# Performance work log

Hardware: AMD Instinct MI355X
Metric: run time of the kernel (lower is better)

## Reference

```python
import jax, jax.numpy as jnp
import numpy as np
from jax import lax

B, N, D = 2, 2048, 1024
H = 16
DH = D // H
EXP = 4
INNER = EXP * D
KS = 3
POWER = 2
LN_EPS = 1e-5


def _layer_norm(x, g, b):
    mu = jnp.mean(x, axis=-1, keepdims=True)
    var = jnp.mean(jnp.square(x - mu), axis=-1, keepdims=True)
    return (x - mu) * lax.rsqrt(var + LN_EPS) * g + b


def setup_inputs() -> dict:
    key = jax.random.key(0)
    ks = jax.random.split(key, 12)
    s = 1.0 / np.sqrt(D)
    si = 1.0 / np.sqrt(INNER)
    return {
        "Q_in": jax.random.normal(ks[0], (B, N, D), jnp.float32),
        "X": jax.random.normal(ks[1], (B, N, D), jnp.float32),
        "Wq": jax.random.normal(ks[2], (D, D), jnp.float32) * s,
        "Wk": jax.random.normal(ks[3], (D, D), jnp.float32) * s,
        "Wv": jax.random.normal(ks[4], (D, D), jnp.float32) * s,
        "Wo": jax.random.normal(ks[5], (D, D), jnp.float32) * s,
        "Wup": jax.random.normal(ks[6], (D, 2 * INNER), jnp.float32) * s,
        "conv_w": jax.random.normal(ks[7], (INNER, 1, KS), jnp.float32) * 0.5,
        "Wdown": jax.random.normal(ks[8], (INNER, D), jnp.float32) * si,
        "g1": jnp.ones((D,), jnp.float32),
        "b1": jnp.zeros((D,), jnp.float32),
        "g2": jnp.ones((D,), jnp.float32),
        "b2": jnp.zeros((D,), jnp.float32),
        "dt": jnp.float32(0.1),
    }


def reference(Q_in, X, Wq, Wk, Wv, Wo, Wup, conv_w, Wdown, g1, b1, g2, b2, dt):
    Bn, Nn, d = Q_in.shape
    # --- attention path: kernelized quadratic attention (relu^power) ---
    Hc = _layer_norm(Q_in, g1, b1) + X                     # [B,N,d]
    def heads(x):
        return x.reshape(Bn, Nn, H, DH).transpose(0, 2, 1, 3)  # [B,H,N,dh]
    Qp = heads(Hc @ Wq)
    Kp = heads(Hc @ Wk)
    Vp = heads(Hc @ Wv)
    PhiQ = jax.nn.elu(Qp) + 1.0
    PhiK = jax.nn.elu(Kp) + 1.0
    W = jnp.einsum("bhnd,bhmd->bhnm", PhiQ, PhiK)          # [B,H,N,N]
    W = jnp.maximum(W, 0.0) ** POWER
    Attr = jnp.einsum("bhnm,bhmd->bhnd", W, Vp)
    Norm = jnp.sum(W, axis=-1, keepdims=True) + 1.0
    m = Attr / Norm - Vp                                   # [B,H,N,dh]
    m_concat = m.transpose(0, 2, 1, 3).reshape(Bn, Nn, d)
    dt_safe = jax.nn.softplus(dt)
    Q_interact = Q_in + dt_safe * (m_concat @ Wo)
    # --- gated depthwise-conv FFN (ConvSwiGLU) ---
    Qn2 = _layer_norm(Q_interact, g2, b2)
    GU = Qn2 @ Wup                                         # [B,N,2*INNER]
    G, U = GU[..., :INNER], GU[..., INNER:]
    Hf = jax.nn.silu(G) * U                                # [B,N,INNER]
    Hf_t = Hf.transpose(0, 2, 1)                           # [B,INNER,N]
    pad = (KS - 1) // 2
    Hc_t = lax.conv_general_dilated(
        Hf_t, conv_w, window_strides=(1,), padding=[(pad, pad)],
        dimension_numbers=("NCH", "OIH", "NCH"), feature_group_count=INNER)
    H_out = Hc_t.transpose(0, 2, 1) @ Wdown
    return Q_interact + H_out
```

## Files before the change

### kernel.cpp

```cpp
#include <hip/hip_runtime.h>

typedef unsigned short u16;
typedef __attribute__((ext_vector_type(8))) __bf16 bf16x8;
typedef __attribute__((ext_vector_type(4))) float f32x4;
typedef __attribute__((ext_vector_type(8))) unsigned short us8v;

__device__ __forceinline__ u16 f2bf(float x){
  union { float f; unsigned u; } v; v.f = x;
  unsigned r = v.u + 0x7fffu + ((v.u >> 16) & 1u);
  return (u16)(r >> 16);
}
__device__ __forceinline__ float bf2f(u16 h){
  union { unsigned u; float f; } v; v.u = ((unsigned)h) << 16;
  return v.f;
}
__device__ __forceinline__ void gld16(const void* g, void* l){
  __builtin_amdgcn_global_load_lds((const __attribute__((address_space(1))) unsigned int*)g,
                                   (__attribute__((address_space(3))) unsigned int*)l, 16, 0, 0);
}

__global__ __launch_bounds__(256) void tr_all(
    const float* __restrict__ Wq, const float* __restrict__ Wk,
    const float* __restrict__ Wv, const float* __restrict__ Wo,
    const float* __restrict__ Wup, const float* __restrict__ Wdown,
    u16* __restrict__ WqkvT, u16* __restrict__ WoT,
    u16* __restrict__ WupT, u16* __restrict__ WdT,
    const float* __restrict__ Qin, const float* __restrict__ X,
    const float* __restrict__ g1, const float* __restrict__ b1,
    u16* __restrict__ HcB)
{
  __shared__ float t[32][33];
  int tx = threadIdx.x, ty = threadIdx.y;
  int id = blockIdx.x;
  if (id >= 16384){
    int row = id - 16384, tid = ty*32 + tx;
    const float4 x = ((const float4*)(Qin + (size_t)row*1024))[tid];
    float s = x.x + x.y + x.z + x.w;
    float sq = x.x*x.x + x.y*x.y + x.z*x.z + x.w*x.w;
    #pragma unroll
    for (int o=32;o>0;o>>=1){ s += __shfl_xor(s, o); sq += __shfl_xor(sq, o); }
    __shared__ float ss[4], ssq[4];
    int wid = tid>>6;
    if ((tid&63)==0){ ss[wid]=s; ssq[wid]=sq; }
    __syncthreads();
    s = ss[0]+ss[1]+ss[2]+ss[3]; sq = ssq[0]+ssq[1]+ssq[2]+ssq[3];
    float mu = s*(1.0f/1024.0f);
    float var = sq*(1.0f/1024.0f) - mu*mu;
    float rstd = rsqrtf(var + 1e-5f);
    float4 xx = ((const float4*)(X + (size_t)row*1024))[tid];
    float4 gv = ((const float4*)g1)[tid];
    float4 bv = ((const float4*)b1)[tid];
    ushort4 o;
    o.x = f2bf((x.x-mu)*rstd*gv.x + bv.x + xx.x);
    o.y = f2bf((x.y-mu)*rstd*gv.y + bv.y + xx.y);
    o.z = f2bf((x.z-mu)*rstd*gv.z + bv.z + xx.z);
    o.w = f2bf((x.w-mu)*rstd*gv.w + bv.w + xx.w);
    ((ushort4*)(HcB + (size_t)row*1024))[tid] = o;
    return;
  }
  if (id < 4096){
    int w = id >> 10, b = id & 1023;
    int c0 = (b & 31)*32, r0 = (b >> 5)*32;
    const float* S = (w==0)?Wq:(w==1)?Wk:(w==2)?Wv:Wo;
    u16* D = (w==3)? WoT : (WqkvT + (size_t)w*1024*1024);
    #pragma unroll
    for (int j=0;j<32;j+=8) t[ty+j][tx] = S[(size_t)(r0+ty+j)*1024 + (c0+tx)];
    __syncthreads();
    #pragma unroll
    for (int j=0;j<32;j+=8) D[(size_t)(c0+ty+j)*1024 + (r0+tx)] = f2bf(t[tx][ty+j]);
  } else if (id < 12288){
    int b = id - 4096;
    int c0 = (b & 255)*32, r0 = (b >> 8)*32;
    #pragma unroll
    for (int j=0;j<32;j+=8) t[ty+j][tx] = Wup[(size_t)(r0+ty+j)*8192 + (c0+tx)];
    __syncthreads();
    #pragma unroll
    for (int j=0;j<32;j+=8){
      int c = c0 + ty + j;
      int rdst = (c < 4096) ? ((c>>4)*32 + (c&15)) : (((c-4096)>>4)*32 + 16 + (c&15));
      WupT[(size_t)rdst*1024 + (r0+tx)] = f2bf(t[tx][ty+j]);
    }
  } else {
    int b = id - 12288;
    int c0 = (b & 31)*32, r0 = (b >> 5)*32;
    #pragma unroll
    for (int j=0;j<32;j+=8) t[ty+j][tx] = Wdown[(size_t)(r0+ty+j)*1024 + (c0+tx)];
    __syncthreads();
    #pragma unroll
    for (int j=0;j<32;j+=8) WdT[(size_t)(c0+ty+j)*4096 + (r0+tx)] = f2bf(t[tx][ty+j]);
  }
}

__global__ __launch_bounds__(256) void ln2_kernel(const u16* __restrict__ P,
    const float* __restrict__ Qin, const float* __restrict__ dtp,
    const float* __restrict__ g, const float* __restrict__ b,
    float* __restrict__ Qint, u16* __restrict__ Qn2){
  int row = blockIdx.x, tid = threadIdx.x;
  float sp = log1pf(__expf(dtp[0]));
  size_t off = (size_t)row*1024;
  ushort4 p0 = ((const ushort4*)(P + off))[tid];
  ushort4 p1 = ((const ushort4*)(P + 4194304 + off))[tid];
  float4 q  = ((const float4*)(Qin + off))[tid];
  float4 x;
  x.x = q.x + sp*(bf2f(p0.x)+bf2f(p1.x)); x.y = q.y + sp*(bf2f(p0.y)+bf2f(p1.y));
  x.z = q.z + sp*(bf2f(p0.z)+bf2f(p1.z)); x.w = q.w + sp*(bf2f(p0.w)+bf2f(p1.w));
  ((float4*)(Qint + off))[tid] = x;
  float s = x.x + x.y + x.z + x.w;
  float sq = x.x*x.x + x.y*x.y + x.z*x.z + x.w*x.w;
  #pragma unroll
  for (int o=32;o>0;o>>=1){ s += __shfl_xor(s, o); sq += __shfl_xor(sq, o); }
  __shared__ float ss[4], ssq[4];
  int wid = tid>>6;
  if ((tid&63)==0){ ss[wid]=s; ssq[wid]=sq; }
  __syncthreads();
  s = ss[0]+ss[1]+ss[2]+ss[3]; sq = ssq[0]+ssq[1]+ssq[2]+ssq[3];
  float mu = s*(1.0f/1024.0f);
  float var = sq*(1.0f/1024.0f) - mu*mu;
  float rstd = rsqrtf(var + 1e-5f);
  float4 gv = ((const float4*)g)[tid];
  float4 bv = ((const float4*)b)[tid];
  ushort4 o;
  o.x = f2bf((x.x-mu)*rstd*gv.x + bv.x);
  o.y = f2bf((x.y-mu)*rstd*gv.y + bv.y);
  o.z = f2bf((x.z-mu)*rstd*gv.z + bv.z);
  o.w = f2bf((x.w-mu)*rstd*gv.w + bv.w);
  ((ushort4*)(Qn2 + off))[tid] = o;
}

__global__ __launch_bounds__(256, 3) void gemm_qkv(
    const u16* __restrict__ A, const u16* __restrict__ Bt, void* __restrict__ Op)
{
  __shared__ u16 As[128*64];
  __shared__ u16 Bs[128*64];
  const int tid = threadIdx.x, wid = tid>>6, lane = tid&63;
  const int g = lane>>4, l = lane&15, l7 = l&7;
  const int row0 = blockIdx.x*128, col0 = blockIdx.y*128;
  const int wr = (wid&1)*64, wc = (wid>>1)*64;
  f32x4 acc[4][4] = {};
  for (int k0 = 0; k0 < 1024; k0 += 64){
    __syncthreads();
    #pragma unroll
    for (int i=0;i<4;i++){
      int ch0 = i*256 + wid*64;
      int ch = ch0 + lane;
      int r = ch >> 3, c = ch & 7;
      int cs = c ^ (r & 7);
      gld16(A  + (size_t)(row0+r)*1024 + k0 + cs*8, (char*)As + ch0*16);
      gld16(Bt + (size_t)(col0+r)*1024 + k0 + cs*8, (char*)Bs + ch0*16);
    }
    __syncthreads();
    #pragma unroll
    for (int kk=0; kk<2; kk++){
      bf16x8 a[4], b[4];
      #pragma unroll
      for (int i=0;i<4;i++) a[i] = *(const bf16x8*)(As + (wr + i*16 + l)*64 + (((kk*4+g)^l7)*8));
      #pragma unroll
      for (int j=0;j<4;j++) b[j] = *(const bf16x8*)(Bs + (wc + j*16 + l)*64 + (((kk*4+g)^l7)*8));
      #pragma unroll
      for (int i=0;i<4;i++)
        #pragma unroll
        for (int j=0;j<4;j++)
          acc[i][j] = __builtin_amdgcn_mfma_f32_16x16x32_bf16(a[i], b[j], acc[i][j], 0, 0, 0);
    }
  }
  u16* P = (u16*)Op;
  #pragma unroll
  for (int i=0;i<4;i++)
   #pragma unroll
   for (int j=0;j<4;j++){
     int col = col0 + wc + j*16 + l;
     int qk = col >> 10, c = col & 1023;
     int h = c >> 6, d = c & 63;
     int rowb = row0 + wr + i*16 + g*4;
     int bb = rowb >> 11, n = rowb & 2047;
     if (qk == 2){
       ushort4 vs;
       vs.x = f2bf(acc[i][j][0]); vs.y = f2bf(acc[i][j][1]);
       vs.z = f2bf(acc[i][j][2]); vs.w = f2bf(acc[i][j][3]);
       *(ushort4*)(P + (size_t)8388608 + (((size_t)(bb*16 + h))*64 + d)*2048 + n) = vs;
     } else {
       #pragma unroll
       for (int r=0;r<4;r++){
         float v = acc[i][j][r];
         float phi = v > 0.f ? v + 1.f : __expf(v);
         P[(size_t)qk*4194304 + (((size_t)(bb*16 + h))*2048 + (n+r))*64 + d] = f2bf(phi);
       }
     }
   }
}

__global__ __launch_bounds__(256, 2) void gemm_wide_up(
    const u16* __restrict__ A, const u16* __restrict__ Bt, u16* __restrict__ Op)
{
  __shared__ u16 As[256*64];
  __shared__ u16 Bs[128*64];
  const int tid = threadIdx.x, wid = tid>>6, lane = tid&63;
  const int g = lane>>4, l = lane&15, l7 = l&7;
  const int bid = blockIdx.x;
  const int bx = bid & 15;
  const int by = (bid>>7)*8 + ((bid>>4) & 7);
  const int row0 = bx*256, col0 = by*128;
  const int wr = (wid&1)*128, wc = (wid>>1)*64;
  f32x4 acc[8][4] = {};
  for (int k0 = 0; k0 < 1024; k0 += 64){
    __syncthreads();
    #pragma unroll
    for (int i=0;i<8;i++){
      int ch0 = i*256 + wid*64;
      int ch = ch0 + lane;
      int r = ch >> 3, c = ch & 7;
      int cs = c ^ (r & 7);
      gld16(A + (size_t)(row0+r)*1024 + k0 + cs*8, (char*)As + ch0*16);
    }
    #pragma unroll
    for (int i=0;i<4;i++){
      int ch0 = i*256 + wid*64;
      int ch = ch0 + lane;
      int r = ch >> 3, c = ch & 7;
      int cs = c ^ (r & 7);
      gld16(Bt + (size_t)(col0+r)*1024 + k0 + cs*8, (char*)Bs + ch0*16);
    }
    __syncthreads();
    #pragma unroll
    for (int kk=0; kk<2; kk++){
      bf16x8 a[8], b[4];
      #pragma unroll
      for (int i=0;i<8;i++) a[i] = *(const bf16x8*)(As + (wr + i*16 + l)*64 + (((kk*4+g)^l7)*8));
      #pragma unroll
      for (int j=0;j<4;j++) b[j] = *(const bf16x8*)(Bs + (wc + j*16 + l)*64 + (((kk*4+g)^l7)*8));
      #pragma unroll
      for (int i=0;i<8;i++)
        #pragma unroll
        for (int j=0;j<4;j++)
          acc[i][j] = __builtin_amdgcn_mfma_f32_16x16x32_bf16(a[i], b[j], acc[i][j], 0, 0, 0);
    }
  }
  #pragma unroll
  for (int i=0;i<8;i++)
   #pragma unroll
   for (int jj=0;jj<4;jj+=2)
    #pragma unroll
    for (int r=0;r<4;r++){
      int row = row0 + wr + i*16 + g*4 + r;
      int pair = (col0 + wc + jj*16) >> 5;
      float G = acc[i][jj][r], U = acc[i][jj+1][r];
      float hf = G/(1.f+__expf(-G))*U;
      Op[(size_t)row*4096 + pair*16 + l] = f2bf(hf);
    }
}

__global__ __launch_bounds__(256, 3) void gemm_part(
    const u16* __restrict__ A, const u16* __restrict__ Bt,
    int Nc, int K, int Ks, u16* __restrict__ Op)
{
  __shared__ u16 As[128*64];
  __shared__ u16 Bs[128*64];
  const int tid = threadIdx.x, wid = tid>>6, lane = tid&63;
  const int g = lane>>4, l = lane&15, l7 = l&7;
  const int row0 = blockIdx.x*128, col0 = blockIdx.y*128;
  const int kbase = blockIdx.z*Ks;
  const int wr = (wid&1)*64, wc = (wid>>1)*64;
  f32x4 acc[4][4] = {};
  for (int k0 = kbase; k0 < kbase + Ks; k0 += 64){
    __syncthreads();
    #pragma unroll
    for (int i=0;i<4;i++){
      int ch0 = i*256 + wid*64;
      int ch = ch0 + lane;
      int r = ch >> 3, c = ch & 7;
      int cs = c ^ (r & 7);
      gld16(A  + (size_t)(row0+r)*K + k0 + cs*8, (char*)As + ch0*16);
      gld16(Bt + (size_t)(col0+r)*K + k0 + cs*8, (char*)Bs + ch0*16);
    }
    __syncthreads();
    #pragma unroll
    for (int kk=0; kk<2; kk++){
      bf16x8 a[4], b[4];
      #pragma unroll
      for (int i=0;i<4;i++) a[i] = *(const bf16x8*)(As + (wr + i*16 + l)*64 + (((kk*4+g)^l7)*8));
      #pragma unroll
      for (int j=0;j<4;j++) b[j] = *(const bf16x8*)(Bs + (wc + j*16 + l)*64 + (((kk*4+g)^l7)*8));
      #pragma unroll
      for (int i=0;i<4;i++)
        #pragma unroll
        for (int j=0;j<4;j++)
          acc[i][j] = __builtin_amdgcn_mfma_f32_16x16x32_bf16(a[i], b[j], acc[i][j], 0, 0, 0);
    }
  }
  u16* P = Op + (size_t)blockIdx.z*4194304;
  #pragma unroll
  for (int i=0;i<4;i++)
   #pragma unroll
   for (int j=0;j<4;j++)
    #pragma unroll
    for (int r=0;r<4;r++){
      int row = row0 + wr + i*16 + g*4 + r;
      int col = col0 + wc + j*16 + l;
      P[(size_t)row*Nc + col] = f2bf(acc[i][j][r]);
    }
}

__global__ __launch_bounds__(256) void reduce_out(const float* __restrict__ Qint,
    const u16* __restrict__ P, float* __restrict__ out){
  size_t i = (size_t)blockIdx.x*256 + threadIdx.x;
  float4 a  = ((const float4*)Qint)[i];
  ushort4 p0 = ((const ushort4*)P)[i];
  ushort4 p1 = ((const ushort4*)(P + 4194304))[i];
  float4 o;
  o.x = a.x + bf2f(p0.x) + bf2f(p1.x); o.y = a.y + bf2f(p0.y) + bf2f(p1.y);
  o.z = a.z + bf2f(p0.z) + bf2f(p1.z); o.w = a.w + bf2f(p0.w) + bf2f(p1.w);
  ((float4*)out)[i] = o;
}

__global__ __launch_bounds__(256, 2) void attn_kernel(
    const u16* __restrict__ PhiQ, const u16* __restrict__ PhiK,
    const u16* __restrict__ Vt, u16* __restrict__ Mb)
{
  __shared__ u16 sK[2][128][32];
  __shared__ u16 sV[4][64][32];
  __shared__ u16 sW[128*128];
  const int tid = threadIdx.x, wid = tid>>6, lane = tid&63;
  const int g = lane>>4, l = lane&15;
  const int l3 = l & 3;
  const int q0 = blockIdx.x*128, bh = blockIdx.y;
  const u16* Q  = PhiQ + (size_t)bh*2048*64;
  const u16* Kb = PhiK + (size_t)bh*2048*64;
  const u16* V  = Vt   + (size_t)bh*64*2048;
  bf16x8 bq[8][2];
  #pragma unroll
  for (int ct=0;ct<8;ct++)
    #pragma unroll
    for (int ks=0;ks<2;ks++)
      bq[ct][ks] = *(const bf16x8*)(Q + (size_t)(q0 + ct*16 + l)*64 + ks*32 + g*8);
  f32x4 accO[2][4] = {};
  float rsum[8] = {0.f,0.f,0.f,0.f,0.f,0.f,0.f,0.f};
  for (int m0 = 0; m0 < 2048; m0 += 128){
    __syncthreads();
    #pragma unroll
    for (int ks=0; ks<2; ks++)
      #pragma unroll
      for (int i=0;i<2;i++){
        int ch0 = i*256 + wid*64;
        int ch = ch0 + lane;
        int r = ch >> 2, q = ch & 3;
        int qs = q ^ (r & 3);
        gld16(Kb + (size_t)(m0+r)*64 + ks*32 + qs*8, (char*)&sK[ks][0][0] + ch0*16);
      }
    #pragma unroll
    for (int c=0; c<4; c++){
      int ch0 = wid*64;
      int ch = ch0 + lane;
      int d = ch >> 2, q = ch & 3;
      int qs = q ^ (d & 3);
      gld16(V + (size_t)d*2048 + m0 + c*32 + qs*8, (char*)&sV[c][0][0] + ch0*16);
    }
    __syncthreads();
    f32x4 st[2][8] = {};
    bf16x8 ak[2][2];
    #pragma unroll
    for (int rt=0;rt<2;rt++)
      #pragma unroll
      for (int ks=0;ks<2;ks++)
        ak[rt][ks] = *(const bf16x8*)&sK[ks][wid*32 + rt*16 + l][(g^l3)*8];
    #pragma unroll
    for (int ct=0;ct<8;ct++){
      #pragma unroll
      for (int ks=0;ks<2;ks++){
        st[0][ct] = __builtin_amdgcn_mfma_f32_16x16x32_bf16(ak[0][ks], bq[ct][ks], st[0][ct], 0,0,0);
        st[1][ct] = __builtin_amdgcn_mfma_f32_16x16x32_bf16(ak[1][ks], bq[ct][ks], st[1][ct], 0,0,0);
      }
    }
    #pragma unroll
    for (int ct=0;ct<8;ct++){
      float part = 0.f;
      #pragma unroll
      for (int rt=0;rt<2;rt++){
        float s0 = fmaxf(st[rt][ct][0], 0.f), s1 = fmaxf(st[rt][ct][1], 0.f);
        float s2 = fmaxf(st[rt][ct][2], 0.f), s3 = fmaxf(st[rt][ct][3], 0.f);
        float w0 = s0*s0, w1 = s1*s1, w2 = s2*s2, w3 = s3*s3;
        part += w0 + w1 + w2 + w3;
        int n = ct*16 + l;
        int mblk = wid*4 + rt*2 + (g>>1);
        ushort4 w4;
        w4.x = f2bf(w0); w4.y = f2bf(w1); w4.z = f2bf(w2); w4.w = f2bf(w3);
        *(ushort4*)(sW + n*128 + ((mblk ^ l)*8) + (g&1)*4) = w4;
      }
      rsum[ct] += part;
    }
    __syncthreads();
    #pragma unroll
    for (int ks=0;ks<4;ks++){
      int n0 = wid*32 + l, n1 = wid*32 + 16 + l;
      bf16x8 aw0 = *(const bf16x8*)(sW + n0*128 + (((ks*4+g) ^ (n0&15))*8));
      bf16x8 aw1 = *(const bf16x8*)(sW + n1*128 + (((ks*4+g) ^ (n1&15))*8));
      #pragma unroll
      for (int ct=0;ct<4;ct++){
        bf16x8 bv = *(const bf16x8*)&sV[ks][ct*16 + l][(g^l3)*8];
        accO[0][ct] = __builtin_amdgcn_mfma_f32_16x16x32_bf16(aw0, bv, accO[0][ct], 0,0,0);
        accO[1][ct] = __builtin_amdgcn_mfma_f32_16x16x32_bf16(aw1, bv, accO[1][ct], 0,0,0);
      }
    }
  }
  __syncthreads();
  float* sRS = (float*)sW;
  float* sNorm = ((float*)sW) + 512;
  #pragma unroll
  for (int ct=0;ct<8;ct++){
    float v = rsum[ct];
    v += __shfl_xor(v, 16);
    v += __shfl_xor(v, 32);
    rsum[ct] = v;
  }
  if (g == 0){
    #pragma unroll
    for (int ct=0;ct<8;ct++) sRS[wid*128 + ct*16 + l] = rsum[ct];
  }
  __syncthreads();
  if (tid < 128) sNorm[tid] = sRS[tid] + sRS[128+tid] + sRS[256+tid] + sRS[384+tid] + 1.0f;
  __syncthreads();
  const int bb = bh >> 4, h = bh & 15;
  #pragma unroll
  for (int rt=0;rt<2;rt++)
   #pragma unroll
   for (int ct=0;ct<4;ct++)
    #pragma unroll
    for (int r=0;r<4;r++){
      int n = wid*32 + rt*16 + g*4 + r;
      int d = ct*16 + l;
      float norm = sNorm[n];
      float vv = bf2f(V[(size_t)d*2048 + q0 + n]);
      float mv = accO[rt][ct][r]/norm - vv;
      Mb[((size_t)(bb*2048) + q0 + n)*1024 + h*64 + d] = f2bf(mv);
    }
}

__global__ __launch_bounds__(256) void conv_kernel(const u16* __restrict__ Hf, const float* __restrict__ w,
                                                   u16* __restrict__ Cv){
  int row = blockIdx.y;
  int n = row & 2047;
  int c0 = (blockIdx.x*256 + threadIdx.x)*8;
  us8v h0 = {0,0,0,0,0,0,0,0}, h2 = {0,0,0,0,0,0,0,0};
  us8v h1 = *(const us8v*)(Hf + (size_t)row*4096 + c0);
  if (n > 0)    h0 = *(const us8v*)(Hf + (size_t)(row-1)*4096 + c0);
  if (n < 2047) h2 = *(const us8v*)(Hf + (size_t)(row+1)*4096 + c0);
  us8v o;
  #pragma unroll
  for (int e=0;e<8;e++){
    int c = c0 + e;
    float acc = bf2f(h0[e])*w[c*3+0] + bf2f(h1[e])*w[c*3+1] + bf2f(h2[e])*w[c*3+2];
    o[e] = f2bf(acc);
  }
  *(us8v*)(Cv + (size_t)row*4096 + c0) = o;
}

extern "C" void kernel_launch(void* const* d_in, const int* in_sizes, int n_in,
                              void* d_out, int out_size, void* d_ws, size_t ws_size,
                              hipStream_t stream)
{
  const float* Q_in  = (const float*)d_in[0];
  const float* X     = (const float*)d_in[1];
  const float* Wq    = (const float*)d_in[2];
  const float* Wk    = (const float*)d_in[3];
  const float* Wv    = (const float*)d_in[4];
  const float* Wo    = (const float*)d_in[5];
  const float* Wup   = (const float*)d_in[6];
  const float* convw = (const float*)d_in[7];
  const float* Wdown = (const float*)d_in[8];
  const float* g1    = (const float*)d_in[9];
  const float* b1    = (const float*)d_in[10];
  const float* g2    = (const float*)d_in[11];
  const float* b2    = (const float*)d_in[12];
  const float* dt    = (const float*)d_in[13];
  float* out = (float*)d_out;

  char* ws = (char*)d_ws;
  const size_t MB = (size_t)1 << 20;
  u16* HcB   = (u16*)(ws + 0*MB);
  u16* WqkvT = (u16*)(ws + 8*MB);
  u16* WoT   = (u16*)(ws + 14*MB);
  u16* PhiQ  = (u16*)(ws + 16*MB);
  u16* Vt    = (u16*)(ws + 32*MB);
  u16* Mb    = (u16*)(ws + 40*MB);
  u16* Po    = (u16*)(ws + 48*MB);
  u16* WupT  = (u16*)(ws + 80*MB);
  u16* WdT   = (u16*)(ws + 96*MB);
  float* Qint = (float*)(ws + 104*MB);
  u16* Qn2   = (u16*)(ws + 120*MB);
  u16* Hf    = (u16*)(ws + 0*MB);
  u16* Cv    = (u16*)(ws + 40*MB);
  u16* Pd    = (u16*)(ws + 0*MB);
  u16* PhiK  = PhiQ + 4194304;

  tr_all<<<20480, dim3(32, 8), 0, stream>>>(Wq, Wk, Wv, Wo, Wup, Wdown,
                                            WqkvT, WoT, WupT, WdT,
                                            Q_in, X, g1, b1, HcB);

  gemm_qkv<<<dim3(32, 24), 256, 0, stream>>>(HcB, WqkvT, PhiQ);

  attn_kernel<<<dim3(16, 32), 256, 0, stream>>>(PhiQ, PhiK, Vt, Mb);

  gemm_part<<<dim3(32, 8, 2), 256, 0, stream>>>(Mb, WoT, 1024, 1024, 512, Po);

  ln2_kernel<<<4096, 256, 0, stream>>>(Po, Q_in, dt, g2, b2, Qint, Qn2);

  gemm_wide_up<<<1024, 256, 0, stream>>>(Qn2, WupT, Hf);

  conv_kernel<<<dim3(2, 4096), 256, 0, stream>>>(Hf, convw, Cv);

  gemm_part<<<dim3(32, 8, 2), 256, 0, stream>>>(Cv, WdT, 1024, 4096, 2048, Pd);
  reduce_out<<<4096, 256, 0, stream>>>(Qint, Pd, out);
}
```

Baseline: 407.9 us.

## Double-buffer the up-projection GEMM with a 256x256 tile and 512 threads

Reworks the gate/up GEMM to use 512-thread blocks computing 256x256 output tiles. The A and B tiles are double-buffered in LDS, with staggered global-to-LDS prefetches and explicit vmcnt waits, so loads overlap MFMA work instead of sitting between two barriers. It also remaps block ids across XCDs and raises wave priority around the MFMA section. The change targets memory latency and barrier stalls, at the cost of 128KB of LDS per block, which limits occupancy to one block per CU.

```diff
diff --git a/kernel.cpp b/kernel.cpp
--- a/kernel.cpp
+++ b/kernel.cpp
@@ -189,52 +189,78 @@
    }
 }
 
-__global__ __launch_bounds__(256, 2) void gemm_wide_up(
+__global__ __launch_bounds__(512, 2) void gemm_wide_up(
     const u16* __restrict__ A, const u16* __restrict__ Bt, u16* __restrict__ Op)
 {
-  __shared__ u16 As[256*64];
-  __shared__ u16 Bs[128*64];
+  __shared__ __attribute__((aligned(16))) u16 As[2][256*64];
+  __shared__ __attribute__((aligned(16))) u16 Bs[2][256*64];
   const int tid = threadIdx.x, wid = tid>>6, lane = tid&63;
   const int g = lane>>4, l = lane&15, l7 = l&7;
   const int bid = blockIdx.x;
-  const int bx = bid & 15;
-  const int by = (bid>>7)*8 + ((bid>>4) & 7);
-  const int row0 = bx*256, col0 = by*128;
+  const int lid = (bid & 7)*64 + (bid >> 3);
+  const int bx = lid & 15, by = lid >> 4;
+  const int row0 = bx*256, col0 = by*256;
   const int wr = (wid&1)*128, wc = (wid>>1)*64;
+  const int rb = tid >> 3;
+  const int csx = (tid & 7) ^ (rb & 7);
+  const u16* Asrc = A  + (size_t)(row0 + rb)*1024 + csx*8;
+  const u16* Bsrc = Bt + (size_t)(col0 + rb)*1024 + csx*8;
   f32x4 acc[8][4] = {};
-  for (int k0 = 0; k0 < 1024; k0 += 64){
-    __syncthreads();
-    #pragma unroll
-    for (int i=0;i<8;i++){
-      int ch0 = i*256 + wid*64;
-      int ch = ch0 + lane;
-      int r = ch >> 3, c = ch & 7;
-      int cs = c ^ (r & 7);
-      gld16(A + (size_t)(row0+r)*1024 + k0 + cs*8, (char*)As + ch0*16);
-    }
-    #pragma unroll
-    for (int i=0;i<4;i++){
-      int ch0 = i*256 + wid*64;
-      int ch = ch0 + lane;
-      int r = ch >> 3, c = ch & 7;
-      int cs = c ^ (r & 7);
-      gld16(Bt + (size_t)(col0+r)*1024 + k0 + cs*8, (char*)Bs + ch0*16);
-    }
-    __syncthreads();
+
+#define STAGE_A(buf, kt) do { \
+  _Pragma("unroll") \
+  for (int i_=0;i_<4;i_++) \
+    gld16(Asrc + (size_t)i_*64*1024 + (kt), (char*)&As[buf][0] + (i_*512 + wid*64)*16); \
+  } while(0)
+#define STAGE_B(buf, kt) do { \
+  _Pragma("unroll") \
+  for (int i_=0;i_<4;i_++) \
+    gld16(Bsrc + (size_t)i_*64*1024 + (kt), (char*)&Bs[buf][0] + (i_*512 + wid*64)*16); \
+  } while(0)
+
+  STAGE_A(0, 0);
+  STAGE_B(0, 0);
+  STAGE_A(1, 64);
+
+  int cur = 0;
+  for (int t = 0; t < 16; ++t){
+    asm volatile("s_waitcnt vmcnt(4)" ::: "memory");
+    __builtin_amdgcn_s_barrier();
+    __builtin_amdgcn_sched_barrier(0);
+    {
+      int kb = ((t+1 < 16) ? (t+1) : t)*64;
+      STAGE_B(cur^1, kb);
+    }
+    __builtin_amdgcn_sched_barrier(0);
+    const u16* Ac = &As[cur][0];
+    const u16* Bc = &Bs[cur][0];
     #pragma unroll
     for (int kk=0; kk<2; kk++){
       bf16x8 a[8], b[4];
       #pragma unroll
-      for (int i=0;i<8;i++) a[i] = *(const bf16x8*)(As + (wr + i*16 + l)*64 + (((kk*4+g)^l7)*8));
-      #pragma unroll
-      for (int j=0;j<4;j++) b[j] = *(const bf16x8*)(Bs + (wc + j*16 + l)*64 + (((kk*4+g)^l7)*8));
+      for (int i=0;i<8;i++) a[i] = *(const bf16x8*)(Ac + (wr + i*16 + l)*64 + (((kk*4+g)^l7)*8));
+      #pragma unroll
+      for (int j=0;j<4;j++) b[j] = *(const bf16x8*)(Bc + (wc + j*16 + l)*64 + (((kk*4+g)^l7)*8));
+      __builtin_amdgcn_s_setprio(1);
       #pragma unroll
       for (int i=0;i<8;i++)
         #pragma unroll
         for (int j=0;j<4;j++)
           acc[i][j] = __builtin_amdgcn_mfma_f32_16x16x32_bf16(a[i], b[j], acc[i][j], 0, 0, 0);
-    }
-  }
+      __builtin_amdgcn_s_setprio(0);
+    }
+    __builtin_amdgcn_sched_barrier(0);
+    __builtin_amdgcn_s_barrier();
+    __builtin_amdgcn_sched_barrier(0);
+    {
+      int ka = ((t+2 < 16) ? (t+2) : 0)*64;
+      STAGE_A(cur, ka);
+    }
+    cur ^= 1;
+  }
+#undef STAGE_A
+#undef STAGE_B
+
   #pragma unroll
   for (int i=0;i<8;i++)
    #pragma unroll
@@ -503,7 +529,7 @@
 
   ln2_kernel<<<4096, 256, 0, stream>>>(Po, Q_in, dt, g2, b2, Qint, Qn2);
 
-  gemm_wide_up<<<1024, 256, 0, stream>>>(Qn2, WupT, Hf);
+  gemm_wide_up<<<512, 512, 0, stream>>>(Qn2, WupT, Hf);
 
   conv_kernel<<<dim3(2, 4096), 256, 0, stream>>>(Hf, convw, Cv);
 
```

Measured after the change: 408.5 us. No clear change (+0.1%).

## Rewrite up-projection GEMM as 256x256 tile, 8-wave, double-buffered pipelined kernel

Applied to the files above, without the earlier changes.

The up-projection GEMM with its fused SwiGLU epilogue moves from 256x128 tiles on 256 threads to 256x256 tiles on 512 threads. It double-buffers LDS in 64-wide K steps and interleaves async global-to-LDS loads of the next stage with MFMA quadrants, using explicit waitcnt, sched barriers and setprio. The block index remap is also changed for L2 locality. The aim is to hide load latency behind MFMA work and get more operand reuse per tile, at the cost of 128KB of LDS, fewer blocks, and fragile hand-tuned vmcnt accounting.

```diff
diff --git a/kernel.cpp b/kernel.cpp
--- a/kernel.cpp
+++ b/kernel.cpp
@@ -189,64 +189,132 @@
    }
 }
 
-__global__ __launch_bounds__(256, 2) void gemm_wide_up(
+__global__ __launch_bounds__(512, 2) void gemm_wide_up(
     const u16* __restrict__ A, const u16* __restrict__ Bt, u16* __restrict__ Op)
 {
-  __shared__ u16 As[256*64];
-  __shared__ u16 Bs[128*64];
+  __shared__ __attribute__((aligned(16))) u16 As[2][256*64];
+  __shared__ __attribute__((aligned(16))) u16 Bs[2][256*64];
   const int tid = threadIdx.x, wid = tid>>6, lane = tid&63;
   const int g = lane>>4, l = lane&15, l7 = l&7;
+  const int wm = wid>>2, wn = wid&3;
   const int bid = blockIdx.x;
-  const int bx = bid & 15;
-  const int by = (bid>>7)*8 + ((bid>>4) & 7);
-  const int row0 = bx*256, col0 = by*128;
-  const int wr = (wid&1)*128, wc = (wid>>1)*64;
-  f32x4 acc[8][4] = {};
-  for (int k0 = 0; k0 < 1024; k0 += 64){
-    __syncthreads();
-    #pragma unroll
-    for (int i=0;i<8;i++){
-      int ch0 = i*256 + wid*64;
-      int ch = ch0 + lane;
-      int r = ch >> 3, c = ch & 7;
-      int cs = c ^ (r & 7);
-      gld16(A + (size_t)(row0+r)*1024 + k0 + cs*8, (char*)As + ch0*16);
-    }
+  const int lid = (bid & 7)*64 + (bid >> 3);
+  const int bx = lid & 15, by = lid >> 4;
+  const int row0 = bx*256, col0 = by*256;
+  const int rA = tid >> 3;
+  const int cs = (tid & 7) ^ (rA & 7);
+  const u16* A0p = A  + (size_t)(row0 + rA)*1024 + cs*8;
+  const u16* A1p = A  + (size_t)(row0 + 64 + rA)*1024 + cs*8;
+  const u16* B0p = Bt + (size_t)(col0 + rA)*1024 + cs*8;
+  const u16* B1p = Bt + (size_t)(col0 + 64 + rA)*1024 + cs*8;
+  const int d0 = (wid*64)*16;
+  const int d1 = (512 + wid*64)*16;
+  const int kc0 = (g ^ l7)*8, kc1 = ((4+g) ^ l7)*8;
+  const int awo = (wm*64 + l)*64;
+  const int bwo = (wn*32 + l)*64;
+
+#define STG_A(buf, half, T) do{ \
+  gld16(A0p + (size_t)(half)*131072 + (size_t)(T)*64, (char*)&As[buf][0] + (half)*16384 + d0); \
+  gld16(A1p + (size_t)(half)*131072 + (size_t)(T)*64, (char*)&As[buf][0] + (half)*16384 + d1); }while(0)
+#define STG_B(buf, half, T) do{ \
+  gld16(B0p + (size_t)(half)*131072 + (size_t)(T)*64, (char*)&Bs[buf][0] + (half)*16384 + d0); \
+  gld16(B1p + (size_t)(half)*131072 + (size_t)(T)*64, (char*)&Bs[buf][0] + (half)*16384 + d1); }while(0)
+#define VMW do{ asm volatile("s_waitcnt vmcnt(10)" ::: "memory"); __builtin_amdgcn_sched_barrier(0); }while(0)
+#define BAR do{ __builtin_amdgcn_sched_barrier(0); __builtin_amdgcn_s_barrier(); __builtin_amdgcn_sched_barrier(0); }while(0)
+#define LGW do{ asm volatile("s_waitcnt lgkmcnt(0)" ::: "memory"); __builtin_amdgcn_sched_barrier(0); }while(0)
+#define MFMA_Q(QM,QN,AV,BV) do{ \
+  __builtin_amdgcn_s_setprio(1); \
+  _Pragma("unroll") \
+  for (int kk=0;kk<2;kk++) \
+    _Pragma("unroll") \
+    for (int i=0;i<4;i++) \
+      _Pragma("unroll") \
+      for (int j=0;j<2;j++) \
+        acc[QM][QN][i][j] = __builtin_amdgcn_mfma_f32_16x16x32_bf16(AV[i][kk], BV[j][kk], acc[QM][QN][i][j], 0,0,0); \
+  __builtin_amdgcn_s_setprio(0); }while(0)
+
+  f32x4 acc[2][2][4][2] = {};
+  bf16x8 a0[4][2], a1[4][2], b0[2][2], b1[2][2];
+
+  STG_A(0, 0, 0);
+  STG_B(0, 0, 0);
+  STG_A(0, 1, 0);
+  STG_B(0, 1, 0);
+  STG_A(1, 0, 1);
+  STG_B(1, 0, 1);
+  STG_A(1, 1, 1);
+  VMW;
+  BAR;
+
+  #pragma unroll 2
+  for (int t = 0; t < 16; ++t){
+    const int c = t & 1;
+    const u16* Ac = &As[c][0];
+    const u16* Bc = &Bs[c][0];
+    const int T1 = (t < 15) ? t+1 : 14;
+    const int T2 = (t < 14) ? t+2 : t;
     #pragma unroll
     for (int i=0;i<4;i++){
-      int ch0 = i*256 + wid*64;
-      int ch = ch0 + lane;
-      int r = ch >> 3, c = ch & 7;
-      int cs = c ^ (r & 7);
-      gld16(Bt + (size_t)(col0+r)*1024 + k0 + cs*8, (char*)Bs + ch0*16);
-    }
-    __syncthreads();
-    #pragma unroll
-    for (int kk=0; kk<2; kk++){
-      bf16x8 a[8], b[4];
-      #pragma unroll
-      for (int i=0;i<8;i++) a[i] = *(const bf16x8*)(As + (wr + i*16 + l)*64 + (((kk*4+g)^l7)*8));
-      #pragma unroll
-      for (int j=0;j<4;j++) b[j] = *(const bf16x8*)(Bs + (wc + j*16 + l)*64 + (((kk*4+g)^l7)*8));
-      #pragma unroll
-      for (int i=0;i<8;i++)
-        #pragma unroll
-        for (int j=0;j<4;j++)
-          acc[i][j] = __builtin_amdgcn_mfma_f32_16x16x32_bf16(a[i], b[j], acc[i][j], 0, 0, 0);
-    }
-  }
-  #pragma unroll
-  for (int i=0;i<8;i++)
+      a0[i][0] = *(const bf16x8*)(Ac + awo + i*1024 + kc0);
+      a0[i][1] = *(const bf16x8*)(Ac + awo + i*1024 + kc1);
+    }
+    #pragma unroll
+    for (int j=0;j<2;j++){
+      b0[j][0] = *(const bf16x8*)(Bc + bwo + j*1024 + kc0);
+      b0[j][1] = *(const bf16x8*)(Bc + bwo + j*1024 + kc1);
+    }
+    STG_B(c^1, 1, T1);
+    VMW;
+    BAR; LGW;
+    MFMA_Q(0,0,a0,b0);
+    BAR;
+    #pragma unroll
+    for (int i=0;i<4;i++){
+      a1[i][0] = *(const bf16x8*)(Ac + 8192 + awo + i*1024 + kc0);
+      a1[i][1] = *(const bf16x8*)(Ac + 8192 + awo + i*1024 + kc1);
+    }
+    STG_A(c, 0, T2);
+    VMW;
+    BAR; LGW;
+    MFMA_Q(1,0,a1,b0);
+    BAR;
+    #pragma unroll
+    for (int j=0;j<2;j++){
+      b1[j][0] = *(const bf16x8*)(Bc + 8192 + bwo + j*1024 + kc0);
+      b1[j][1] = *(const bf16x8*)(Bc + 8192 + bwo + j*1024 + kc1);
+    }
+    STG_B(c, 0, T2);
+    BAR; LGW;
+    MFMA_Q(1,1,a1,b1);
+    BAR;
+    STG_A(c, 1, T2);
+    VMW;
+    BAR;
+    MFMA_Q(0,1,a0,b1);
+    BAR;
+  }
+  asm volatile("s_waitcnt vmcnt(0)" ::: "memory");
+#undef STG_A
+#undef STG_B
+#undef VMW
+#undef BAR
+#undef LGW
+#undef MFMA_Q
+
+  #pragma unroll
+  for (int Qm=0;Qm<2;Qm++)
    #pragma unroll
-   for (int jj=0;jj<4;jj+=2)
-    #pragma unroll
-    for (int r=0;r<4;r++){
-      int row = row0 + wr + i*16 + g*4 + r;
-      int pair = (col0 + wc + jj*16) >> 5;
-      float G = acc[i][jj][r], U = acc[i][jj+1][r];
-      float hf = G/(1.f+__expf(-G))*U;
-      Op[(size_t)row*4096 + pair*16 + l] = f2bf(hf);
-    }
+   for (int Qn=0;Qn<2;Qn++)
+    #pragma unroll
+    for (int i=0;i<4;i++)
+     #pragma unroll
+     for (int r=0;r<4;r++){
+       int row = row0 + Qm*128 + wm*64 + i*16 + g*4 + r;
+       int pair = (col0 + Qn*128 + wn*32) >> 5;
+       float G = acc[Qm][Qn][i][0][r], U = acc[Qm][Qn][i][1][r];
+       float hf = G/(1.f+__expf(-G))*U;
+       Op[(size_t)row*4096 + pair*16 + l] = f2bf(hf);
+     }
 }
 
 __global__ __launch_bounds__(256, 3) void gemm_part(
@@ -503,7 +571,7 @@
 
   ln2_kernel<<<4096, 256, 0, stream>>>(Po, Q_in, dt, g2, b2, Qint, Qn2);
 
-  gemm_wide_up<<<1024, 256, 0, stream>>>(Qn2, WupT, Hf);
+  gemm_wide_up<<<512, 512, 0, stream>>>(Qn2, WupT, Hf);
 
   conv_kernel<<<dim3(2, 4096), 256, 0, stream>>>(Hf, convw, Cv);
 
```

Measured after the change: 412.0 us. No clear change (+1.0%).
